# Kernel tuning notes

Measured on AMD Instinct MI355X. Metric: run time of the kernel, lower is better.

The kernel has to match this reference:

```python
import jax, jax.numpy as jnp
import numpy as np

B, L, CIN = 128, 2048, 38
D, S, PD, FEAT, FD, NH = 64, 32, 32, 64, 128, 4


def _ln(x, g, b, eps=1e-5):
    m = jnp.mean(x, axis=-1, keepdims=True)
    v = jnp.var(x, axis=-1, keepdims=True)
    return (x - m) / jnp.sqrt(v + eps) * g + b


def _gelu(x):
    return jax.nn.gelu(x, approximate=False)


def setup_inputs():
    key = jax.random.key(0)
    ks = jax.random.split(key, 20)
    w = lambda k, shape: jax.random.normal(k, shape, jnp.float32) * 0.02
    z = lambda *s: jnp.zeros(s, jnp.float32)
    inp = {}
    inp['x'] = jax.random.normal(ks[0], (B, L, CIN), jnp.float32)
    # physics core
    inp['Wv'] = w(ks[1], (3, CIN)); inp['bv'] = z(3)
    inp['Wr'] = w(ks[2], (3, CIN)); inp['br'] = z(3)
    inp['Wpe'] = w(ks[3], (5, PD)); inp['bpe'] = z(PD)
    inp['g_pe'] = jnp.ones((PD,), jnp.float32); inp['be_pe'] = z(PD)
    # mamba stream: in-proj + LN, then selective-scan block
    inp['Wmi'] = w(ks[4], (CIN, D)); inp['bmi'] = z(D)
    inp['g_m'] = jnp.ones((D,), jnp.float32); inp['b_m'] = z(D)
    inp['A_log'] = jnp.tile(jnp.log(jnp.arange(1, S + 1, dtype=jnp.float32)), (D, 1))
    inp['Wdt'] = w(ks[5], (1, D)); inp['bdt'] = z(D)
    inp['Wxp'] = w(ks[6], (D, 2 * S)); inp['bxp'] = z(2 * S)
    inp['Wmo'] = w(ks[7], (D, D)); inp['bmo'] = z(D)
    # champion feature extractor (stand-in: mean-pool + linear to champion_feat_dim)
    inp['Wch'] = w(ks[8], (CIN, FEAT)); inp['bch'] = z(FEAT)
    # alignment + attention fusion + classifier
    inp['Wac'] = w(ks[9], (FEAT, FD)); inp['bac'] = z(FD)
    inp['Wamp'] = w(ks[10], (PD + D, FD)); inp['bamp'] = z(FD)
    inp['Wq'] = w(ks[11], (FD, FD)); inp['bq'] = z(FD)
    inp['Wk'] = w(ks[12], (FD, FD)); inp['bk'] = z(FD)
    inp['Wva'] = w(ks[13], (FD, FD)); inp['bva'] = z(FD)
    inp['Wo'] = w(ks[14], (FD, FD)); inp['bo'] = z(FD)
    inp['Wc1'] = w(ks[15], (FD, 64)); inp['bc1'] = z(64)
    inp['Wc2'] = w(ks[16], (64, 1)); inp['bc2'] = z(1)
    return inp


def reference(x, Wv, bv, Wr, br, Wpe, bpe, g_pe, be_pe, Wmi, bmi, g_m, b_m,
              A_log, Wdt, bdt, Wxp, bxp, Wmo, bmo, Wch, bch, Wac, bac,
              Wamp, bamp, Wq, bq, Wk, bk, Wva, bva, Wo, bo, Wc1, bc1, Wc2, bc2):
    Bn, Ln, _ = x.shape
    # ---------- TulparPhysicsCore (conv1d k=1 == per-position linear) ----------
    v_vec = jnp.clip(jnp.einsum('blc,oc->blo', x, Wv) + bv, -15.0, 15.0)      # [B,L,3]
    r_vec = jnp.clip(jax.nn.softplus(jnp.einsum('blc,oc->blo', x, Wr) + br), 0.1, 3000.0)
    v_mag = jnp.linalg.norm(v_vec, axis=-1)                                    # [B,L]
    r_mag = jnp.linalg.norm(r_vec, axis=-1)
    energy = v_mag ** 2 / 2.0 - 1.0 / r_mag
    ediff = jnp.concatenate([jnp.zeros((Bn, 1), x.dtype), energy[:, 1:] - energy[:, :-1]], axis=1)
    praw = jnp.stack([v_mag, r_mag, energy, ediff, r_mag / v_mag], axis=-1)    # [B,L,5]
    phys = _gelu(_ln(praw @ Wpe + bpe, g_pe, be_pe))                           # [B,L,PD]
    # ---------- mamba stream: Linear -> LN -> GELU -> selective scan ----------
    h = _gelu(_ln(x @ Wmi + bmi, g_m, b_m))                                    # [B,L,D]
    A = -jnp.exp(A_log)                                                        # [D,S]
    dt = jax.nn.softplus(h[:, :, 0:1] @ Wdt + bdt)                             # [B,L,D]
    Bm, Cm = jnp.split(h @ Wxp + bxp, 2, axis=-1)                              # [B,L,S] each

    def step(state, inp_t):
        dt_t, h_t, B_t, C_t = inp_t                                            # [B,D],[B,D],[B,S],[B,S]
        dA = jnp.exp(A[None] * dt_t[:, :, None])                               # [B,D,S]
        state = dA * state + dt_t[:, :, None] * h_t[:, :, None] * B_t[:, None, :]
        y = (state * C_t[:, None, :]).sum(-1)                                  # [B,D]
        return state, y

    init = jnp.zeros((Bn, D, S), x.dtype)
    xs = (dt.transpose(1, 0, 2), h.transpose(1, 0, 2),
          Bm.transpose(1, 0, 2), Cm.transpose(1, 0, 2))
    _, ys = jax.lax.scan(step, init, xs)                                       # [L,B,D]
    mamba = ys.transpose(1, 0, 2) @ Wmo + bmo                                  # [B,L,D]
    # ---------- fusion ----------
    kv = jnp.concatenate([phys, mamba], axis=-1) @ Wamp + bamp                 # [B,L,FD]
    feat = x.mean(axis=1) @ Wch + bch                                          # [B,FEAT] (champion.get_features)
    q = (feat @ Wac + bac)[:, None, :]                                         # [B,1,FD]
    Dh = FD // NH
    qh = (q @ Wq + bq).reshape(Bn, 1, NH, Dh).transpose(0, 2, 1, 3)            # [B,H,1,Dh]
    kh = (kv @ Wk + bk).reshape(Bn, Ln, NH, Dh).transpose(0, 2, 1, 3)          # [B,H,L,Dh]
    vh = (kv @ Wva + bva).reshape(Bn, Ln, NH, Dh).transpose(0, 2, 1, 3)
    scores = jnp.einsum('bhqd,bhkd->bhqk', qh, kh) * (1.0 / np.sqrt(Dh))
    att = jax.nn.softmax(scores, axis=-1)                                      # [B,H,1,L]
    o = jnp.einsum('bhqk,bhkd->bhqd', att, vh).transpose(0, 2, 1, 3).reshape(Bn, 1, FD)
    o = (o @ Wo + bo)[:, 0, :]                                                 # [B,FD]
    # ---------- classifier (dropout = identity in eval) ----------
    return _gelu(o @ Wc1 + bc1) @ Wc2 + bc2                                    # [B,1]
```

## Files before the change

kernel.cpp:

```cpp
#include <hip/hip_runtime.h>
#include <math.h>

constexpr int B   = 128;
constexpr int L   = 2048;
constexpr int CIN = 38;
constexpr int D   = 64;
constexpr int S   = 32;
constexpr int PD  = 32;
constexpr int FEAT= 64;
constexpr int FD  = 128;
constexpr int NH  = 4;
constexpr int DH  = 32;

constexpr int NC  = 32;
constexpr int CL  = 64;
constexpr int TT  = 16;
constexpr int NCH = 16;
constexpr int CHL = 128;
constexpr int NBLK = (B*L)/64;

constexpr size_t SZ_H   = (size_t)B*L*D;
constexpr size_t SZ_BC  = (size_t)B*L*S;
constexpr size_t SZ_PH  = (size_t)B*L*PD;
constexpr size_t SZ_ST  = (size_t)B*NC*D*S;
constexpr size_t SZ_SDT = (size_t)B*NC*D;

constexpr size_t OFF_H    = 0;
constexpr size_t OFF_BC   = OFF_H   + SZ_H;
constexpr size_t OFF_CC   = OFF_BC  + SZ_BC;
constexpr size_t OFF_PHYS = OFF_CC  + SZ_BC;
constexpr size_t OFF_ST   = OFF_PHYS+ SZ_PH;
constexpr size_t OFF_SDT  = OFF_ST  + SZ_ST;
constexpr size_t OFF_XM   = OFF_SDT + SZ_SDT;
constexpr size_t OFF_PA   = OFF_XM  + (size_t)NBLK*CIN;
constexpr size_t OFF_PY   = OFF_PA  + (size_t)B*NH*PD;
constexpr size_t OFF_C0   = OFF_PY  + (size_t)B*NH*D;
constexpr size_t OFF_PMS  = OFF_ST;
constexpr size_t OFF_PCTX = OFF_ST + 32768;

__device__ __forceinline__ float fast_rcp(float v) {
#if __has_builtin(__builtin_amdgcn_rcpf)
    return __builtin_amdgcn_rcpf(v);
#else
    return 1.f / v;
#endif
}
__device__ __forceinline__ float sp_fast(float z) {
    return fmaxf(z, 0.f) + __logf(1.f + __expf(-fabsf(z)));
}
__device__ __forceinline__ float gelu_fast(float v) {
    const float u = v * 0.70710678118654752f;
    const float a = fabsf(u);
    const float t = fast_rcp(fmaf(0.3275911f, a, 1.f));
    const float poly = t*(0.254829592f + t*(-0.284496736f + t*(1.421413741f
                        + t*(-1.453152027f + t*1.061405429f))));
    const float e = __expf(-a*a);
    const float erfa = fmaf(-poly, e, 1.f);
    const float erfu = copysignf(erfa, u);
    return 0.5f * v * (1.f + erfu);
}

__device__ __forceinline__ float energy_at(const float* __restrict__ xr,
    const float* __restrict__ Wv, const float* __restrict__ bv,
    const float* __restrict__ Wr, const float* __restrict__ br)
{
    float vm2 = 0.f, rm2 = 0.f;
    #pragma unroll
    for (int o = 0; o < 3; o++) {
        float a = bv[o], rr = br[o];
        #pragma unroll
        for (int c = 0; c < CIN; c++) {
            a  = fmaf(xr[c], Wv[o*CIN + c], a);
            rr = fmaf(xr[c], Wr[o*CIN + c], rr);
        }
        a  = fminf(fmaxf(a, -15.f), 15.f);
        rr = fminf(fmaxf(sp_fast(rr), 0.1f), 3000.f);
        vm2 += a*a; rm2 += rr*rr;
    }
    const float rmag = sqrtf(rm2);
    return 0.5f*vm2 - 1.f/rmag;
}

__global__ __launch_bounds__(256, 6) void k_pre(
    const float* __restrict__ x,
    const float* __restrict__ Wv,  const float* __restrict__ bv,
    const float* __restrict__ Wr,  const float* __restrict__ br,
    const float* __restrict__ Wpe, const float* __restrict__ bpe,
    const float* __restrict__ gpe, const float* __restrict__ bepe,
    const float* __restrict__ Wmi, const float* __restrict__ bmi,
    const float* __restrict__ gm,  const float* __restrict__ bm,
    const float* __restrict__ Wxp, const float* __restrict__ bxp,
    float* __restrict__ hws, float* __restrict__ bcw,
    float* __restrict__ ccw, float* __restrict__ phw,
    float* __restrict__ xpart)
{
    __shared__ __align__(16) float smem[4928];
    const int tid = threadIdx.x;
    const int g   = __builtin_amdgcn_readfirstlane(tid) >> 6;
    const int row = tid & 63;
    const int r0  = blockIdx.x * 64;
    const int p   = r0 + row;
    const int l   = p & (L - 1);
    const float* xr = x + (size_t)p * CIN;

    float xv[CIN];
    #pragma unroll
    for (int c = 0; c < CIN; c++) xv[c] = xr[c];

    if (g == 0) {
        #pragma unroll
        for (int c = 0; c < CIN; c++) smem[row*40 + c] = xv[c];
    }
    __syncthreads();

    if (g == 0) {
        float vm2 = 0.f, rm2 = 0.f;
        #pragma unroll
        for (int o = 0; o < 3; o++) {
            float a = bv[o], rr = br[o];
            #pragma unroll
            for (int c = 0; c < CIN; c++) {
                a  = fmaf(xv[c], Wv[o*CIN + c], a);
                rr = fmaf(xv[c], Wr[o*CIN + c], rr);
            }
            a  = fminf(fmaxf(a, -15.f), 15.f);
            rr = fminf(fmaxf(sp_fast(rr), 0.1f), 3000.f);
            vm2 += a*a; rm2 += rr*rr;
        }
        const float vmag = sqrtf(vm2), rmag = sqrtf(rm2);
        const float energy = 0.5f*vm2 - 1.f/rmag;
        float eprev = __shfl(energy, (row == 0) ? 0 : row - 1, 64);
        if (row == 0 && l > 0) eprev = energy_at(xr - CIN, Wv, bv, Wr, br);
        const float ediff = (l == 0) ? 0.f : (energy - eprev);
        smem[2720 + row*5 + 0] = vmag;
        smem[2720 + row*5 + 1] = rmag;
        smem[2720 + row*5 + 2] = energy;
        smem[2720 + row*5 + 3] = ediff;
        smem[2720 + row*5 + 4] = rmag / vmag;
    }
    if (tid >= 128 && tid < 128 + 4*CIN) {
        const int idx = tid - 128;
        const int c2 = idx >> 2, sub = idx & 3;
        float s2 = 0.f;
        #pragma unroll
        for (int r2 = 0; r2 < 16; r2++) s2 += smem[(sub*16 + r2)*40 + c2];
        smem[3552 + idx] = s2;
    }
    __syncthreads();
    if (tid < CIN)
        xpart[(size_t)blockIdx.x*CIN + tid] = smem[3552 + 4*tid] + smem[3552 + 4*tid + 1]
                                            + smem[3552 + 4*tid + 2] + smem[3552 + 4*tid + 3];

    {
        float pr[5];
        #pragma unroll
        for (int j = 0; j < 5; j++) pr[j] = smem[2720 + row*5 + j];
        float peo[8]; float ls = 0.f, lq = 0.f;
        #pragma unroll
        for (int i = 0; i < 8; i++) {
            const int ii = 8*g + i;
            float a = bpe[ii];
            #pragma unroll
            for (int k = 0; k < 5; k++) a = fmaf(pr[k], Wpe[k*PD + ii], a);
            peo[i] = a; ls += a; lq += a*a;
        }
        smem[3040 + g*64 + row] = ls;
        smem[3296 + g*64 + row] = lq;
        __syncthreads();
        float mu = 0.f, sq = 0.f;
        #pragma unroll
        for (int w = 0; w < 4; w++) {
            mu += smem[3040 + w*64 + row];
            sq += smem[3296 + w*64 + row];
        }
        mu *= (1.f/PD);
        const float var = fmaxf(sq*(1.f/PD) - mu*mu, 0.f);
        const float rstd = rsqrtf(var + 1e-5f);
        #pragma unroll
        for (int k = 0; k < 2; k++) {
            float4 q;
            q.x = gelu_fast((peo[4*k+0]-mu)*rstd*gpe[8*g+4*k+0] + bepe[8*g+4*k+0]);
            q.y = gelu_fast((peo[4*k+1]-mu)*rstd*gpe[8*g+4*k+1] + bepe[8*g+4*k+1]);
            q.z = gelu_fast((peo[4*k+2]-mu)*rstd*gpe[8*g+4*k+2] + bepe[8*g+4*k+2]);
            q.w = gelu_fast((peo[4*k+3]-mu)*rstd*gpe[8*g+4*k+3] + bepe[8*g+4*k+3]);
            *(float4*)&smem[row*36 + 8*g + 4*k] = q;
        }
    }
    __syncthreads();
    {
        float* pb = phw + (size_t)r0 * PD;
        #pragma unroll
        for (int k = 0; k < 2; k++) {
            const int flat = k*1024 + tid*4;
            const int rr = flat >> 5, cc = flat & 31;
            *(float4*)&pb[flat] = *(const float4*)&smem[rr*36 + cc];
        }
    }
    __syncthreads();

    float hq[16];
    {
        float sum = 0.f, sumsq = 0.f;
        #pragma unroll
        for (int jj = 0; jj < 4; jj++) {
            #pragma unroll
            for (int j2 = 0; j2 < 4; j2++) {
                const int d = 16*g + 4*jj + j2;
                float a = bmi[d];
                #pragma unroll
                for (int c = 0; c < CIN; c++) a = fmaf(xv[c], Wmi[c*D + d], a);
                hq[4*jj + j2] = a; sum += a; sumsq += a*a;
            }
        }
        smem[4352 + g*64 + row] = sum;
        smem[4608 + g*64 + row] = sumsq;
    }
    __syncthreads();
    {
        float s = 0.f, sq = 0.f;
        #pragma unroll
        for (int w = 0; w < 4; w++) {
            s  += smem[4352 + w*64 + row];
            sq += smem[4608 + w*64 + row];
        }
        const float mu = s * (1.f/D);
        const float var = fmaxf(sq*(1.f/D) - mu*mu, 0.f);
        const float rstd = rsqrtf(var + 1e-5f);
        #pragma unroll
        for (int jj = 0; jj < 4; jj++) {
            const int d0 = 16*g + 4*jj;
            float4 q;
            q.x = gelu_fast(fmaf((hq[4*jj+0]-mu)*rstd, gm[d0+0], bm[d0+0]));
            q.y = gelu_fast(fmaf((hq[4*jj+1]-mu)*rstd, gm[d0+1], bm[d0+1]));
            q.z = gelu_fast(fmaf((hq[4*jj+2]-mu)*rstd, gm[d0+2], bm[d0+2]));
            q.w = gelu_fast(fmaf((hq[4*jj+3]-mu)*rstd, gm[d0+3], bm[d0+3]));
            *(float4*)&smem[row*68 + d0] = q;
        }
    }
    __syncthreads();
    {
        float* hb = hws + (size_t)r0 * D;
        #pragma unroll
        for (int k = 0; k < 4; k++) {
            const int flat = k*1024 + tid*4;
            const int rr = flat >> 6, cc = flat & 63;
            *(float4*)&hb[flat] = *(const float4*)&smem[rr*68 + cc];
        }
    }

    float acc[16];
    {
        const int j0 = 16*g;
        #pragma unroll
        for (int j = 0; j < 16; j++) acc[j] = bxp[j0 + j];
        #pragma unroll 1
        for (int dg = 0; dg < 16; dg++) {
            const float4 hv4 = *(const float4*)&smem[row*68 + 4*dg];
            const float hv[4] = {hv4.x, hv4.y, hv4.z, hv4.w};
            #pragma unroll
            for (int j2 = 0; j2 < 4; j2++) {
                const int d = 4*dg + j2;
                #pragma unroll
                for (int j = 0; j < 16; j++)
                    acc[j] = fmaf(hv[j2], Wxp[d*2*S + j0 + j], acc[j]);
            }
        }
    }
    __syncthreads();
    {
        float* dst = (g < 2) ? &smem[row*36 + 16*g] : &smem[2304 + row*36 + 16*(g-2)];
        #pragma unroll
        for (int k = 0; k < 4; k++)
            *(float4*)&dst[4*k] = make_float4(acc[4*k], acc[4*k+1], acc[4*k+2], acc[4*k+3]);
    }
    __syncthreads();
    {
        float* bb = bcw + (size_t)r0 * S;
        float* cb = ccw + (size_t)r0 * S;
        #pragma unroll
        for (int k = 0; k < 2; k++) {
            const int flat = k*1024 + tid*4;
            const int rr = flat >> 5, cc = flat & 31;
            *(float4*)&bb[flat] = *(const float4*)&smem[rr*36 + cc];
            *(float4*)&cb[flat] = *(const float4*)&smem[2304 + rr*36 + cc];
        }
    }
}

__global__ __launch_bounds__(64) void k_q(
    const float* __restrict__ xpart,
    const float* __restrict__ Wch, const float* __restrict__ bch,
    const float* __restrict__ Wac, const float* __restrict__ bac,
    const float* __restrict__ Wq,  const float* __restrict__ bq,
    const float* __restrict__ Wk,  const float* __restrict__ bk,
    const float* __restrict__ Wamp,const float* __restrict__ bamp,
    const float* __restrict__ Wmo, const float* __restrict__ bmo,
    float* __restrict__ pA, float* __restrict__ pY, float* __restrict__ c0w)
{
    const int bh = blockIdx.x;
    const int b = bh >> 2, h = bh & 3;
    const int t = threadIdx.x;
    __shared__ float xmL[CIN];
    __shared__ float featL[FEAT], qL[FD], qvL[FD], qkL[FD], pML[D];
    __shared__ float qbL;
    if (t < CIN) {
        float s2 = 0.f;
        #pragma unroll 4
        for (int g2 = 0; g2 < 32; g2++) s2 += xpart[((size_t)b*32 + g2)*CIN + t];
        xmL[t] = s2 * (1.f/L);
    }
    __syncthreads();
    {
        float a = bch[t];
        #pragma unroll
        for (int c = 0; c < CIN; c++) a = fmaf(xmL[c], Wch[c*FEAT + t], a);
        featL[t] = a;
    }
    __syncthreads();
    #pragma unroll
    for (int k2 = 0; k2 < 2; k2++) {
        const int f = t + k2*64;
        float a = bac[f];
        #pragma unroll
        for (int j = 0; j < FEAT; j++) a = fmaf(featL[j], Wac[j*FD + f], a);
        qL[f] = a;
    }
    __syncthreads();
    #pragma unroll
    for (int k2 = 0; k2 < 2; k2++) {
        const int f = t + k2*64;
        float a = bq[f];
        #pragma unroll
        for (int j = 0; j < FD; j++) a = fmaf(qL[j], Wq[j*FD + f], a);
        qvL[f] = a;
    }
    __syncthreads();
    #pragma unroll
    for (int k2 = 0; k2 < 2; k2++) {
        const int f = t + k2*64;
        float a = 0.f;
        #pragma unroll
        for (int j = 0; j < DH; j++) a = fmaf(Wk[f*FD + h*DH + j], qvL[h*DH + j], a);
        qkL[f] = a;
    }
    if (t == 0) {
        float a = 0.f;
        for (int j = 0; j < DH; j++) a = fmaf(bk[h*DH + j], qvL[h*DH + j], a);
        qbL = a;
    }
    __syncthreads();
    const float sc = 0.17677669529663688f;
    if (t < PD) {
        float a = 0.f;
        #pragma unroll
        for (int f = 0; f < FD; f++) a = fmaf(Wamp[t*FD + f], qkL[f], a);
        pA[bh*PD + t] = a * sc;
    }
    {
        float a = 0.f;
        #pragma unroll
        for (int f = 0; f < FD; f++) a = fmaf(Wamp[(PD + t)*FD + f], qkL[f], a);
        pML[t] = a;
    }
    __syncthreads();
    {
        float a = 0.f;
        #pragma unroll
        for (int d2 = 0; d2 < D; d2++) a = fmaf(Wmo[t*D + d2], pML[d2], a);
        pY[bh*D + t] = a * sc;
    }
    if (t == 0) {
        float a = qbL;
        for (int f = 0; f < FD; f++)  a = fmaf(bamp[f], qkL[f], a);
        for (int d2 = 0; d2 < D; d2++) a = fmaf(bmo[d2], pML[d2], a);
        c0w[bh] = a * sc;
    }
}

__global__ __launch_bounds__(256) void k_scan1(
    const float* __restrict__ Wdt, const float* __restrict__ bdt,
    const float* __restrict__ hws, const float* __restrict__ bcw,
    float* __restrict__ stw, float* __restrict__ sdtw)
{
    __shared__ __align__(16) float hL[TT*D];
    __shared__ __align__(16) float bL[TT*S];
    __shared__ __align__(16) float uL[TT*D];
    __shared__ __align__(16) float e1L[TT*D];
    __shared__ float sdL[4*D];
    const int bc = blockIdx.x;
    const int b = bc >> 5, c = bc & (NC - 1);
    const int tid = threadIdx.x;
    const int d = tid & 63, w = tid >> 6;
    const float wdt = Wdt[d], bd = bdt[d];
    float st[8];
    #pragma unroll
    for (int k = 0; k < 8; k++) st[k] = 0.f;
    float sumdt = 0.f;
    const size_t row0 = (size_t)b*L + (size_t)c*CL;
    const float* hg = hws + row0*D;
    const float* bg = bcw + row0*S;

    float4 hpre = *(const float4*)&hg[tid*4];
    float4 bpre;
    if (tid < 128) bpre = *(const float4*)&bg[tid*4];

    for (int ts = 0; ts < CL/TT; ts++) {
        *(float4*)&hL[tid*4] = hpre;
        if (tid < 128) *(float4*)&bL[tid*4] = bpre;
        __syncthreads();
        if (ts < CL/TT - 1) {
            hpre = *(const float4*)&hg[(ts+1)*TT*D + tid*4];
            if (tid < 128) bpre = *(const float4*)&bg[(ts+1)*TT*S + tid*4];
        }
        #pragma unroll
        for (int j = 0; j < 4; j++) {
            const int t = 4*w + j;
            const float h0 = hL[t*D];
            const float hd = hL[t*D + d];
            float z = fmaf(h0, wdt, bd);
            z = fminf(fmaxf(z, -30.f), 30.f);
            const float ez = __expf(z);
            const float e1 = fast_rcp(1.f + ez);
            const float dt = -__logf(e1);
            sumdt += dt;
            uL[t*D + d]  = dt * hd;
            e1L[t*D + d] = e1;
        }
        __syncthreads();
        #pragma unroll
        for (int t = 0; t < TT; t++) {
            const float e1 = e1L[t*D + d];
            const float u  = uL[t*D + d];
            const float e2 = e1*e1, e4 = e2*e2, e8 = e4*e4, e16 = e8*e8;
            float pf = e1;
            pf *= (w & 1) ? e8 : 1.f;
            pf *= (w & 2) ? e16 : 1.f;
            float bv[8];
            *(float4*)&bv[0] = *(const float4*)&bL[t*S + 8*w];
            *(float4*)&bv[4] = *(const float4*)&bL[t*S + 8*w + 4];
            #pragma unroll
            for (int k = 0; k < 8; k++) {
                st[k] = fmaf(pf, st[k], u * bv[k]);
                pf *= e1;
            }
        }
        __syncthreads();
    }
    float* F = stw + (size_t)bc*(D*S) + (size_t)(8*w)*D + d;
    #pragma unroll
    for (int k = 0; k < 8; k++) F[k*D] = st[k];
    sdL[w*D + d] = sumdt;
    __syncthreads();
    if (tid < D)
        sdtw[(size_t)bc*D + tid] = sdL[tid] + sdL[D + tid] + sdL[2*D + tid] + sdL[3*D + tid];
}

__global__ __launch_bounds__(256) void k_scan2(float* __restrict__ stw,
                                               const float* __restrict__ sdtw)
{
    const int idx = blockIdx.x*256 + threadIdx.x;
    const int d = idx & 63;
    const int s = (idx >> 6) & (S - 1);
    const int b = idx >> 11;
    const float sp1 = -(float)(s + 1);
    float st = 0.f;
    for (int c = 0; c < NC; c++) {
        float* p2 = stw + (size_t)(b*NC + c)*(D*S) + (size_t)s*D + d;
        const float sdt = sdtw[(size_t)(b*NC + c)*D + d];
        const float F = *p2;
        *p2 = st;
        st = fmaf(__expf(sp1 * sdt), st, F);
    }
}

__global__ __launch_bounds__(256) void k_scan3(
    const float* __restrict__ Wdt, const float* __restrict__ bdt,
    float* __restrict__ hws,
    const float* __restrict__ bcw, const float* __restrict__ ccw,
    const float* __restrict__ stw)
{
    __shared__ __align__(16) float hL[TT*D];
    __shared__ __align__(16) float bL[TT*S];
    __shared__ __align__(16) float cL[TT*S];
    __shared__ __align__(16) float uL[TT*D];
    __shared__ __align__(16) float e1L[TT*D];
    __shared__ __align__(16) float ypL[4*TT*D];
    const int bc = blockIdx.x;
    const int b = bc >> 5, c = bc & (NC - 1);
    const int tid = threadIdx.x;
    const int d = tid & 63, w = tid >> 6;
    const float wdt = Wdt[d], bd = bdt[d];
    float st[8];
    {
        const float* initp = stw + (size_t)bc*(D*S) + (size_t)(8*w)*D + d;
        #pragma unroll
        for (int k = 0; k < 8; k++) st[k] = initp[k*D];
    }
    const size_t row0 = (size_t)b*L + (size_t)c*CL;
    float* hg = hws + row0*D;
    const float* bg = bcw + row0*S;
    const float* cg = ccw + row0*S;

    float4 hpre = *(const float4*)&hg[tid*4];
    float4 bcpre;
    if (tid < 128) bcpre = *(const float4*)&bg[tid*4];
    else           bcpre = *(const float4*)&cg[(tid-128)*4];

    for (int ts = 0; ts < CL/TT; ts++) {
        *(float4*)&hL[tid*4] = hpre;
        if (tid < 128) *(float4*)&bL[tid*4] = bcpre;
        else           *(float4*)&cL[(tid-128)*4] = bcpre;
        __syncthreads();
        if (ts < CL/TT - 1) {
            hpre = *(const float4*)&hg[(ts+1)*TT*D + tid*4];
            if (tid < 128) bcpre = *(const float4*)&bg[(ts+1)*TT*S + tid*4];
            else           bcpre = *(const float4*)&cg[(ts+1)*TT*S + (tid-128)*4];
        }
        #pragma unroll
        for (int j = 0; j < 4; j++) {
            const int t = 4*w + j;
            const float h0 = hL[t*D];
            const float hd = hL[t*D + d];
            float z = fmaf(h0, wdt, bd);
            z = fminf(fmaxf(z, -30.f), 30.f);
            const float ez = __expf(z);
            const float e1 = fast_rcp(1.f + ez);
            const float dt = -__logf(e1);
            uL[t*D + d]  = dt * hd;
            e1L[t*D + d] = e1;
        }
        __syncthreads();
        #pragma unroll
        for (int t = 0; t < TT; t++) {
            const float e1 = e1L[t*D + d];
            const float u  = uL[t*D + d];
            const float e2 = e1*e1, e4 = e2*e2, e8 = e4*e4, e16 = e8*e8;
            float pf = e1;
            pf *= (w & 1) ? e8 : 1.f;
            pf *= (w & 2) ? e16 : 1.f;
            float bv[8], cv[8];
            *(float4*)&bv[0] = *(const float4*)&bL[t*S + 8*w];
            *(float4*)&bv[4] = *(const float4*)&bL[t*S + 8*w + 4];
            *(float4*)&cv[0] = *(const float4*)&cL[t*S + 8*w];
            *(float4*)&cv[4] = *(const float4*)&cL[t*S + 8*w + 4];
            float y = 0.f;
            #pragma unroll
            for (int k = 0; k < 8; k++) {
                st[k] = fmaf(pf, st[k], u * bv[k]);
                y = fmaf(st[k], cv[k], y);
                pf *= e1;
            }
            ypL[(w*TT + t)*D + d] = y;
        }
        __syncthreads();
        {
            const int flat = tid*4;
            float4 a  = *(const float4*)&ypL[flat];
            const float4 p1 = *(const float4*)&ypL[TT*D + flat];
            const float4 p2 = *(const float4*)&ypL[2*TT*D + flat];
            const float4 p3 = *(const float4*)&ypL[3*TT*D + flat];
            a.x += p1.x + p2.x + p3.x;
            a.y += p1.y + p2.y + p3.y;
            a.z += p1.z + p2.z + p3.z;
            a.w += p1.w + p2.w + p3.w;
            *(float4*)&hg[(size_t)(ts*TT)*D + flat] = a;
        }
        __syncthreads();
    }
}

__global__ __launch_bounds__(256) void k_att(
    const float* __restrict__ phw, const float* __restrict__ yw,
    const float* __restrict__ pA,  const float* __restrict__ pY,
    const float* __restrict__ c0w,
    float* __restrict__ pms, float* __restrict__ pctx)
{
    const int blk = blockIdx.x;
    const int b = blk >> 4, c = blk & (NCH - 1);
    const int tid = threadIdx.x;
    __shared__ __align__(16) float phL[CHL*36];
    __shared__ __align__(16) float yL[CHL*68];
    __shared__ float scL[NH*CHL];
    __shared__ float wL[CHL*NH];
    __shared__ __align__(16) float sPA[NH*PD];
    __shared__ __align__(16) float sPY[NH*D];
    __shared__ float sC0[NH];

    if (tid < NH*PD) sPA[tid] = pA[(size_t)b*NH*PD + tid];
    sPY[tid] = pY[(size_t)b*NH*D + tid];
    if (tid < NH) sC0[tid] = c0w[b*NH + tid];

    const float* phg = phw + ((size_t)b*L + (size_t)c*CHL)*PD;
    #pragma unroll
    for (int it = 0; it < 4; it++) {
        const int flat = it*1024 + tid*4;
        const int row = flat >> 5, col = flat & 31;
        *(float4*)&phL[row*36 + col] = *(const float4*)&phg[flat];
    }
    const float* yg = yw + ((size_t)b*L + (size_t)c*CHL)*D;
    #pragma unroll
    for (int it = 0; it < 8; it++) {
        const int flat = it*1024 + tid*4;
        const int row = flat >> 6, col = flat & 63;
        *(float4*)&yL[row*68 + col] = *(const float4*)&yg[flat];
    }
    __syncthreads();

    #pragma unroll
    for (int it = 0; it < 2; it++) {
        const int item = it*256 + tid;
        const int row = item & (CHL - 1), hh = item >> 7;
        float a = sC0[hh];
        #pragma unroll
        for (int k = 0; k < 8; k++) {
            const float4 pq = *(const float4*)&phL[row*36 + 4*k];
            const float4 aq = *(const float4*)&sPA[hh*PD + 4*k];
            a = fmaf(pq.x, aq.x, a); a = fmaf(pq.y, aq.y, a);
            a = fmaf(pq.z, aq.z, a); a = fmaf(pq.w, aq.w, a);
        }
        #pragma unroll
        for (int k = 0; k < 16; k++) {
            const float4 yq = *(const float4*)&yL[row*68 + 4*k];
            const float4 aq = *(const float4*)&sPY[hh*D + 4*k];
            a = fmaf(yq.x, aq.x, a); a = fmaf(yq.y, aq.y, a);
            a = fmaf(yq.z, aq.z, a); a = fmaf(yq.w, aq.w, a);
        }
        scL[hh*CHL + row] = a;
    }
    __syncthreads();

    {
        const int hh = tid >> 6, lane = tid & 63;
        const float v0 = scL[hh*CHL + lane], v1 = scL[hh*CHL + lane + 64];
        float mx = fmaxf(v0, v1);
        #pragma unroll
        for (int o = 32; o > 0; o >>= 1) mx = fmaxf(mx, __shfl_xor(mx, o, 64));
        const float e0 = __expf(v0 - mx), e1 = __expf(v1 - mx);
        wL[lane*NH + hh] = e0;
        wL[(lane + 64)*NH + hh] = e1;
        float sum = e0 + e1;
        #pragma unroll
        for (int o = 32; o > 0; o >>= 1) sum += __shfl_xor(sum, o, 64);
        if (lane == 0) {
            pms[((size_t)blk*NH + hh)*2 + 0] = mx;
            pms[((size_t)blk*NH + hh)*2 + 1] = sum;
        }
    }
    __syncthreads();

    for (int item = tid; item < NH*(PD + D); item += 256) {
        const int hh = item / (PD + D), e = item % (PD + D);
        const float* fb; int stp;
        if (e < PD) { fb = &phL[e]; stp = 36; }
        else        { fb = &yL[e - PD]; stp = 68; }
        float acc = 0.f;
        #pragma unroll 4
        for (int r = 0; r < CHL; r++) acc = fmaf(wL[r*NH + hh], fb[r*stp], acc);
        pctx[((size_t)blk*NH + hh)*(PD + D) + e] = acc;
    }
}

__global__ __launch_bounds__(128) void k_att2(
    const float* __restrict__ pms, const float* __restrict__ pctx,
    const float* __restrict__ Wmo, const float* __restrict__ bmo,
    const float* __restrict__ Wamp,const float* __restrict__ bamp,
    const float* __restrict__ Wva, const float* __restrict__ bva,
    const float* __restrict__ Wo,  const float* __restrict__ bo,
    const float* __restrict__ Wc1, const float* __restrict__ bc1,
    const float* __restrict__ Wc2, const float* __restrict__ bc2,
    float* __restrict__ out)
{
    const int b = blockIdx.x, t = threadIdx.x;
    __shared__ float ctxL[NH][PD + D];
    __shared__ float catL[NH][PD + D];
    __shared__ float ckvL[NH][FD];
    __shared__ float oL[FD], ooL[FD], c1L[64];

    for (int idx = t; idx < NH*(PD + D); idx += 128) {
        const int hh = idx / (PD + D), e = idx % (PD + D);
        float M = -3.0e38f;
        for (int cc = 0; cc < NCH; cc++)
            M = fmaxf(M, pms[((size_t)(b*NCH + cc)*NH + hh)*2]);
        float Ssum = 0.f, acc = 0.f;
        for (int cc = 0; cc < NCH; cc++) {
            const size_t pi = (size_t)(b*NCH + cc)*NH + hh;
            const float f = __expf(pms[pi*2] - M);
            Ssum += pms[pi*2 + 1] * f;
            acc  += f * pctx[pi*(PD + D) + e];
        }
        ctxL[hh][e] = acc / Ssum;
    }
    __syncthreads();
    for (int idx = t; idx < NH*(PD + D); idx += 128) {
        const int hh = idx / (PD + D), i = idx % (PD + D);
        float a;
        if (i < PD) a = ctxL[hh][i];
        else {
            const int d2 = i - PD;
            a = bmo[d2];
            #pragma unroll
            for (int e = 0; e < D; e++) a = fmaf(ctxL[hh][PD + e], Wmo[e*D + d2], a);
        }
        catL[hh][i] = a;
    }
    __syncthreads();
    for (int idx = t; idx < NH*FD; idx += 128) {
        const int hh = idx / FD, f = idx % FD;
        float a = bamp[f];
        #pragma unroll
        for (int i = 0; i < PD + D; i++) a = fmaf(catL[hh][i], Wamp[i*FD + f], a);
        ckvL[hh][f] = a;
    }
    __syncthreads();
    {
        const int hh = t / DH, j = t % DH;
        float a = bva[hh*DH + j];
        #pragma unroll
        for (int f = 0; f < FD; f++) a = fmaf(ckvL[hh][f], Wva[f*FD + hh*DH + j], a);
        oL[t] = a;
    }
    __syncthreads();
    {
        float a = bo[t];
        #pragma unroll
        for (int f = 0; f < FD; f++) a = fmaf(oL[f], Wo[f*FD + t], a);
        ooL[t] = a;
    }
    __syncthreads();
    if (t < 64) {
        float a = bc1[t];
        #pragma unroll
        for (int f = 0; f < FD; f++) a = fmaf(ooL[f], Wc1[f*64 + t], a);
        c1L[t] = gelu_fast(a);
    }
    __syncthreads();
    if (t == 0) {
        float a = bc2[0];
        for (int k2 = 0; k2 < 64; k2++) a = fmaf(c1L[k2], Wc2[k2], a);
        out[b] = a;
    }
}

extern "C" void kernel_launch(void* const* d_in, const int* in_sizes, int n_in,
                              void* d_out, int out_size, void* d_ws, size_t ws_size,
                              hipStream_t stream)
{
    const float* x    = (const float*)d_in[0];
    const float* Wv   = (const float*)d_in[1];
    const float* bv   = (const float*)d_in[2];
    const float* Wr   = (const float*)d_in[3];
    const float* br   = (const float*)d_in[4];
    const float* Wpe  = (const float*)d_in[5];
    const float* bpe  = (const float*)d_in[6];
    const float* gpe  = (const float*)d_in[7];
    const float* bepe = (const float*)d_in[8];
    const float* Wmi  = (const float*)d_in[9];
    const float* bmi  = (const float*)d_in[10];
    const float* gm   = (const float*)d_in[11];
    const float* bm   = (const float*)d_in[12];
    const float* Wdt  = (const float*)d_in[14];
    const float* bdt  = (const float*)d_in[15];
    const float* Wxp  = (const float*)d_in[16];
    const float* bxp  = (const float*)d_in[17];
    const float* Wmo  = (const float*)d_in[18];
    const float* bmo  = (const float*)d_in[19];
    const float* Wch  = (const float*)d_in[20];
    const float* bch  = (const float*)d_in[21];
    const float* Wac  = (const float*)d_in[22];
    const float* bac  = (const float*)d_in[23];
    const float* Wamp = (const float*)d_in[24];
    const float* bamp = (const float*)d_in[25];
    const float* Wq   = (const float*)d_in[26];
    const float* bq   = (const float*)d_in[27];
    const float* Wk   = (const float*)d_in[28];
    const float* bk   = (const float*)d_in[29];
    const float* Wva  = (const float*)d_in[30];
    const float* bva  = (const float*)d_in[31];
    const float* Wo   = (const float*)d_in[32];
    const float* bo   = (const float*)d_in[33];
    const float* Wc1  = (const float*)d_in[34];
    const float* bc1  = (const float*)d_in[35];
    const float* Wc2  = (const float*)d_in[36];
    const float* bc2  = (const float*)d_in[37];

    float* ws  = (float*)d_ws;
    float* out = (float*)d_out;

    float* hws  = ws + OFF_H;
    float* bcw  = ws + OFF_BC;
    float* ccw  = ws + OFF_CC;
    float* phw  = ws + OFF_PHYS;
    float* stw  = ws + OFF_ST;
    float* sdtw = ws + OFF_SDT;
    float* xmw  = ws + OFF_XM;
    float* pAw  = ws + OFF_PA;
    float* pYw  = ws + OFF_PY;
    float* c0w  = ws + OFF_C0;
    float* pms  = ws + OFF_PMS;
    float* pctx = ws + OFF_PCTX;

    k_pre<<<dim3(NBLK), dim3(256), 0, stream>>>(x, Wv, bv, Wr, br, Wpe, bpe,
        gpe, bepe, Wmi, bmi, gm, bm, Wxp, bxp, hws, bcw, ccw, phw, xmw);
    k_q<<<dim3(B*NH), dim3(64), 0, stream>>>(xmw, Wch, bch, Wac, bac, Wq, bq,
        Wk, bk, Wamp, bamp, Wmo, bmo, pAw, pYw, c0w);
    k_scan1<<<dim3(B*NC), dim3(256), 0, stream>>>(Wdt, bdt, hws, bcw, stw, sdtw);
    k_scan2<<<dim3((B*S*D)/256), dim3(256), 0, stream>>>(stw, sdtw);
    k_scan3<<<dim3(B*NC), dim3(256), 0, stream>>>(Wdt, bdt, hws, bcw, ccw, stw);
    k_att<<<dim3(B*NCH), dim3(256), 0, stream>>>(phw, hws, pAw, pYw, c0w, pms, pctx);
    k_att2<<<dim3(B), dim3(128), 0, stream>>>(pms, pctx, Wmo, bmo, Wamp, bamp,
        Wva, bva, Wo, bo, Wc1, bc1, Wc2, bc2, out);
}
```

Measured before the change: 459.6 us.

## Fuse chunk-state scan into preprocessing and fuse output scan with attention

```diff
diff --git a/kernel.cpp b/kernel.cpp
--- a/kernel.cpp
+++ b/kernel.cpp
@@ -35,8 +35,6 @@
 constexpr size_t OFF_PA   = OFF_XM  + (size_t)NBLK*CIN;
 constexpr size_t OFF_PY   = OFF_PA  + (size_t)B*NH*PD;
 constexpr size_t OFF_C0   = OFF_PY  + (size_t)B*NH*D;
-constexpr size_t OFF_PMS  = OFF_ST;
-constexpr size_t OFF_PCTX = OFF_ST + 32768;
 
 __device__ __forceinline__ float fast_rcp(float v) {
 #if __has_builtin(__builtin_amdgcn_rcpf)
@@ -81,7 +79,7 @@
     return 0.5f*vm2 - 1.f/rmag;
 }
 
-__global__ __launch_bounds__(256, 6) void k_pre(
+__global__ __launch_bounds__(256, 4) void k_pre(
     const float* __restrict__ x,
     const float* __restrict__ Wv,  const float* __restrict__ bv,
     const float* __restrict__ Wr,  const float* __restrict__ br,
@@ -90,11 +88,15 @@
     const float* __restrict__ Wmi, const float* __restrict__ bmi,
     const float* __restrict__ gm,  const float* __restrict__ bm,
     const float* __restrict__ Wxp, const float* __restrict__ bxp,
+    const float* __restrict__ Wdt, const float* __restrict__ bdt,
     float* __restrict__ hws, float* __restrict__ bcw,
     float* __restrict__ ccw, float* __restrict__ phw,
-    float* __restrict__ xpart)
+    float* __restrict__ xpart, float* __restrict__ stw,
+    float* __restrict__ sdtw)
 {
-    __shared__ __align__(16) float smem[4928];
+    __shared__ __align__(16) float smem[9216];
+    constexpr int TB0 = 4352, TC0 = 6656;
+    constexpr int PH36 = 4352, PR0 = 6656, PS0 = 6976, PQ0 = 7232, XMP = 8960;
     const int tid = threadIdx.x;
     const int g   = __builtin_amdgcn_readfirstlane(tid) >> 6;
     const int row = tid & 63;
@@ -132,11 +134,11 @@
         float eprev = __shfl(energy, (row == 0) ? 0 : row - 1, 64);
         if (row == 0 && l > 0) eprev = energy_at(xr - CIN, Wv, bv, Wr, br);
         const float ediff = (l == 0) ? 0.f : (energy - eprev);
-        smem[2720 + row*5 + 0] = vmag;
-        smem[2720 + row*5 + 1] = rmag;
-        smem[2720 + row*5 + 2] = energy;
-        smem[2720 + row*5 + 3] = ediff;
-        smem[2720 + row*5 + 4] = rmag / vmag;
+        smem[PR0 + row*5 + 0] = vmag;
+        smem[PR0 + row*5 + 1] = rmag;
+        smem[PR0 + row*5 + 2] = energy;
+        smem[PR0 + row*5 + 3] = ediff;
+        smem[PR0 + row*5 + 4] = rmag / vmag;
     }
     if (tid >= 128 && tid < 128 + 4*CIN) {
         const int idx = tid - 128;
@@ -144,17 +146,17 @@
         float s2 = 0.f;
         #pragma unroll
         for (int r2 = 0; r2 < 16; r2++) s2 += smem[(sub*16 + r2)*40 + c2];
-        smem[3552 + idx] = s2;
+        smem[XMP + idx] = s2;
     }
     __syncthreads();
     if (tid < CIN)
-        xpart[(size_t)blockIdx.x*CIN + tid] = smem[3552 + 4*tid] + smem[3552 + 4*tid + 1]
-                                            + smem[3552 + 4*tid + 2] + smem[3552 + 4*tid + 3];
+        xpart[(size_t)blockIdx.x*CIN + tid] = smem[XMP + 4*tid] + smem[XMP + 4*tid + 1]
+                                            + smem[XMP + 4*tid + 2] + smem[XMP + 4*tid + 3];
 
     {
         float pr[5];
         #pragma unroll
-        for (int j = 0; j < 5; j++) pr[j] = smem[2720 + row*5 + j];
+        for (int j = 0; j < 5; j++) pr[j] = smem[PR0 + row*5 + j];
         float peo[8]; float ls = 0.f, lq = 0.f;
         #pragma unroll
         for (int i = 0; i < 8; i++) {
@@ -164,14 +166,14 @@
             for (int k = 0; k < 5; k++) a = fmaf(pr[k], Wpe[k*PD + ii], a);
             peo[i] = a; ls += a; lq += a*a;
         }
-        smem[3040 + g*64 + row] = ls;
-        smem[3296 + g*64 + row] = lq;
+        smem[PS0 + g*64 + row] = ls;
+        smem[PQ0 + g*64 + row] = lq;
         __syncthreads();
         float mu = 0.f, sq = 0.f;
         #pragma unroll
         for (int w = 0; w < 4; w++) {
-            mu += smem[3040 + w*64 + row];
-            sq += smem[3296 + w*64 + row];
+            mu += smem[PS0 + w*64 + row];
+            sq += smem[PQ0 + w*64 + row];
         }
         mu *= (1.f/PD);
         const float var = fmaxf(sq*(1.f/PD) - mu*mu, 0.f);
@@ -183,7 +185,7 @@
             q.y = gelu_fast((peo[4*k+1]-mu)*rstd*gpe[8*g+4*k+1] + bepe[8*g+4*k+1]);
             q.z = gelu_fast((peo[4*k+2]-mu)*rstd*gpe[8*g+4*k+2] + bepe[8*g+4*k+2]);
             q.w = gelu_fast((peo[4*k+3]-mu)*rstd*gpe[8*g+4*k+3] + bepe[8*g+4*k+3]);
-            *(float4*)&smem[row*36 + 8*g + 4*k] = q;
+            *(float4*)&smem[PH36 + row*36 + 8*g + 4*k] = q;
         }
     }
     __syncthreads();
@@ -193,7 +195,7 @@
         for (int k = 0; k < 2; k++) {
             const int flat = k*1024 + tid*4;
             const int rr = flat >> 5, cc = flat & 31;
-            *(float4*)&pb[flat] = *(const float4*)&smem[rr*36 + cc];
+            *(float4*)&pb[flat] = *(const float4*)&smem[PH36 + rr*36 + cc];
         }
     }
     __syncthreads();
@@ -212,16 +214,16 @@
                 hq[4*jj + j2] = a; sum += a; sumsq += a*a;
             }
         }
-        smem[4352 + g*64 + row] = sum;
-        smem[4608 + g*64 + row] = sumsq;
+        smem[PS0 + g*64 + row] = sum;
+        smem[PQ0 + g*64 + row] = sumsq;
     }
     __syncthreads();
     {
         float s = 0.f, sq = 0.f;
         #pragma unroll
         for (int w = 0; w < 4; w++) {
-            s  += smem[4352 + w*64 + row];
-            sq += smem[4608 + w*64 + row];
+            s  += smem[PS0 + w*64 + row];
+            sq += smem[PQ0 + w*64 + row];
         }
         const float mu = s * (1.f/D);
         const float var = fmaxf(sq*(1.f/D) - mu*mu, 0.f);
@@ -266,9 +268,8 @@
             }
         }
     }
-    __syncthreads();
-    {
-        float* dst = (g < 2) ? &smem[row*36 + 16*g] : &smem[2304 + row*36 + 16*(g-2)];
+    {
+        float* dst = (g < 2) ? &smem[TB0 + row*36 + 16*g] : &smem[TC0 + row*36 + 16*(g-2)];
         #pragma unroll
         for (int k = 0; k < 4; k++)
             *(float4*)&dst[4*k] = make_float4(acc[4*k], acc[4*k+1], acc[4*k+2], acc[4*k+3]);
@@ -281,9 +282,45 @@
         for (int k = 0; k < 2; k++) {
             const int flat = k*1024 + tid*4;
             const int rr = flat >> 5, cc = flat & 31;
-            *(float4*)&bb[flat] = *(const float4*)&smem[rr*36 + cc];
-            *(float4*)&cb[flat] = *(const float4*)&smem[2304 + rr*36 + cc];
-        }
+            *(float4*)&bb[flat] = *(const float4*)&smem[TB0 + rr*36 + cc];
+            *(float4*)&cb[flat] = *(const float4*)&smem[TC0 + rr*36 + cc];
+        }
+    }
+
+    {
+        const float wdt = Wdt[row], bd2 = bdt[row];
+        float st[8];
+        #pragma unroll
+        for (int k = 0; k < 8; k++) st[k] = 0.f;
+        float sumdt = 0.f;
+        #pragma unroll 2
+        for (int t = 0; t < CL; t++) {
+            const float h0 = smem[t*68];
+            const float hd = smem[t*68 + row];
+            float z = fmaf(h0, wdt, bd2);
+            z = fminf(fmaxf(z, -30.f), 30.f);
+            const float ez = __expf(z);
+            const float e1 = fast_rcp(1.f + ez);
+            const float dt = -__logf(e1);
+            sumdt += dt;
+            const float u = dt * hd;
+            const float e2 = e1*e1, e4 = e2*e2, e8 = e4*e4, e16 = e8*e8;
+            float pf = e1;
+            pf *= (g & 1) ? e8 : 1.f;
+            pf *= (g & 2) ? e16 : 1.f;
+            float bvv[8];
+            *(float4*)&bvv[0] = *(const float4*)&smem[TB0 + t*36 + 8*g];
+            *(float4*)&bvv[4] = *(const float4*)&smem[TB0 + t*36 + 8*g + 4];
+            #pragma unroll
+            for (int k = 0; k < 8; k++) {
+                st[k] = fmaf(pf, st[k], u * bvv[k]);
+                pf *= e1;
+            }
+        }
+        float* F = stw + (size_t)blockIdx.x*(D*S) + (size_t)(8*g)*D + row;
+        #pragma unroll
+        for (int k = 0; k < 8; k++) F[k*D] = st[k];
+        if (g == 0) sdtw[(size_t)blockIdx.x*D + row] = sumdt;
     }
 }
 
@@ -377,84 +414,6 @@
     }
 }
 
-__global__ __launch_bounds__(256) void k_scan1(
-    const float* __restrict__ Wdt, const float* __restrict__ bdt,
-    const float* __restrict__ hws, const float* __restrict__ bcw,
-    float* __restrict__ stw, float* __restrict__ sdtw)
-{
-    __shared__ __align__(16) float hL[TT*D];
-    __shared__ __align__(16) float bL[TT*S];
-    __shared__ __align__(16) float uL[TT*D];
-    __shared__ __align__(16) float e1L[TT*D];
-    __shared__ float sdL[4*D];
-    const int bc = blockIdx.x;
-    const int b = bc >> 5, c = bc & (NC - 1);
-    const int tid = threadIdx.x;
-    const int d = tid & 63, w = tid >> 6;
-    const float wdt = Wdt[d], bd = bdt[d];
-    float st[8];
-    #pragma unroll
-    for (int k = 0; k < 8; k++) st[k] = 0.f;
-    float sumdt = 0.f;
-    const size_t row0 = (size_t)b*L + (size_t)c*CL;
-    const float* hg = hws + row0*D;
-    const float* bg = bcw + row0*S;
-
-    float4 hpre = *(const float4*)&hg[tid*4];
-    float4 bpre;
-    if (tid < 128) bpre = *(const float4*)&bg[tid*4];
-
-    for (int ts = 0; ts < CL/TT; ts++) {
-        *(float4*)&hL[tid*4] = hpre;
-        if (tid < 128) *(float4*)&bL[tid*4] = bpre;
-        __syncthreads();
-        if (ts < CL/TT - 1) {
-            hpre = *(const float4*)&hg[(ts+1)*TT*D + tid*4];
-            if (tid < 128) bpre = *(const float4*)&bg[(ts+1)*TT*S + tid*4];
-        }
-        #pragma unroll
-        for (int j = 0; j < 4; j++) {
-            const int t = 4*w + j;
-            const float h0 = hL[t*D];
-            const float hd = hL[t*D + d];
-            float z = fmaf(h0, wdt, bd);
-            z = fminf(fmaxf(z, -30.f), 30.f);
-            const float ez = __expf(z);
-            const float e1 = fast_rcp(1.f + ez);
-            const float dt = -__logf(e1);
-            sumdt += dt;
-            uL[t*D + d]  = dt * hd;
-            e1L[t*D + d] = e1;
-        }
-        __syncthreads();
-        #pragma unroll
-        for (int t = 0; t < TT; t++) {
-            const float e1 = e1L[t*D + d];
-            const float u  = uL[t*D + d];
-            const float e2 = e1*e1, e4 = e2*e2, e8 = e4*e4, e16 = e8*e8;
-            float pf = e1;
-            pf *= (w & 1) ? e8 : 1.f;
-            pf *= (w & 2) ? e16 : 1.f;
-            float bv[8];
-            *(float4*)&bv[0] = *(const float4*)&bL[t*S + 8*w];
-            *(float4*)&bv[4] = *(const float4*)&bL[t*S + 8*w + 4];
-            #pragma unroll
-            for (int k = 0; k < 8; k++) {
-                st[k] = fmaf(pf, st[k], u * bv[k]);
-                pf *= e1;
-            }
-        }
-        __syncthreads();
-    }
-    float* F = stw + (size_t)bc*(D*S) + (size_t)(8*w)*D + d;
-    #pragma unroll
-    for (int k = 0; k < 8; k++) F[k*D] = st[k];
-    sdL[w*D + d] = sumdt;
-    __syncthreads();
-    if (tid < D)
-        sdtw[(size_t)bc*D + tid] = sdL[tid] + sdL[D + tid] + sdL[2*D + tid] + sdL[3*D + tid];
-}
-
 __global__ __launch_bounds__(256) void k_scan2(float* __restrict__ stw,
                                                const float* __restrict__ sdtw)
 {
@@ -473,52 +432,66 @@
     }
 }
 
-__global__ __launch_bounds__(256) void k_scan3(
+__global__ __launch_bounds__(256, 4) void k_scan3att(
     const float* __restrict__ Wdt, const float* __restrict__ bdt,
-    float* __restrict__ hws,
-    const float* __restrict__ bcw, const float* __restrict__ ccw,
-    const float* __restrict__ stw)
+    const float* __restrict__ hws, const float* __restrict__ bcw,
+    const float* __restrict__ ccw, const float* __restrict__ phw,
+    const float* __restrict__ pA,  const float* __restrict__ pY,
+    const float* __restrict__ c0w, float* __restrict__ stw)
 {
     __shared__ __align__(16) float hL[TT*D];
     __shared__ __align__(16) float bL[TT*S];
     __shared__ __align__(16) float cL[TT*S];
-    __shared__ __align__(16) float uL[TT*D];
-    __shared__ __align__(16) float e1L[TT*D];
     __shared__ __align__(16) float ypL[4*TT*D];
-    const int bc = blockIdx.x;
-    const int b = bc >> 5, c = bc & (NC - 1);
+    __shared__ __align__(16) float ySub[TT*68];
+    __shared__ __align__(16) float phSub[TT*36];
+    __shared__ float wSub[64];
+    __shared__ float mh[NH], lh[NH], alphaL[NH];
+    __shared__ __align__(16) float sPA[NH*PD];
+    __shared__ __align__(16) float sPY[NH*D];
+    __shared__ float sC0[NH];
+    const int blk = blockIdx.x;
+    const int b = blk >> 4, c = blk & (NCH - 1);
     const int tid = threadIdx.x;
     const int d = tid & 63, w = tid >> 6;
     const float wdt = Wdt[d], bd = bdt[d];
     float st[8];
     {
-        const float* initp = stw + (size_t)bc*(D*S) + (size_t)(8*w)*D + d;
+        const float* initp = stw + (size_t)(b*NC + 2*c)*(D*S) + (size_t)(8*w)*D + d;
         #pragma unroll
         for (int k = 0; k < 8; k++) st[k] = initp[k*D];
     }
-    const size_t row0 = (size_t)b*L + (size_t)c*CL;
-    float* hg = hws + row0*D;
+    if (tid < NH*PD) sPA[tid] = pA[(size_t)b*NH*PD + tid];
+    sPY[tid] = pY[(size_t)b*NH*D + tid];
+    if (tid < NH) { sC0[tid] = c0w[b*NH + tid]; mh[tid] = -3.0e38f; lh[tid] = 0.f; }
+    float acc0 = 0.f, acc1 = 0.f;
+    const size_t row0 = (size_t)b*L + (size_t)c*CHL;
+    const float* hg = hws + row0*D;
     const float* bg = bcw + row0*S;
     const float* cg = ccw + row0*S;
-
+    const float* pg = phw + row0*PD;
     float4 hpre = *(const float4*)&hg[tid*4];
-    float4 bcpre;
-    if (tid < 128) bcpre = *(const float4*)&bg[tid*4];
-    else           bcpre = *(const float4*)&cg[(tid-128)*4];
-
-    for (int ts = 0; ts < CL/TT; ts++) {
+    float4 bcpre = (tid < 128) ? *(const float4*)&bg[tid*4]
+                               : *(const float4*)&cg[(tid-128)*4];
+    float2 ppre = *(const float2*)&pg[tid*2];
+
+    for (int ts = 0; ts < CHL/TT; ts++) {
         *(float4*)&hL[tid*4] = hpre;
         if (tid < 128) *(float4*)&bL[tid*4] = bcpre;
         else           *(float4*)&cL[(tid-128)*4] = bcpre;
+        {
+            const int flat = tid*2;
+            *(float2*)&phSub[(flat >> 5)*36 + (flat & 31)] = ppre;
+        }
         __syncthreads();
-        if (ts < CL/TT - 1) {
+        if (ts < CHL/TT - 1) {
             hpre = *(const float4*)&hg[(ts+1)*TT*D + tid*4];
-            if (tid < 128) bcpre = *(const float4*)&bg[(ts+1)*TT*S + tid*4];
-            else           bcpre = *(const float4*)&cg[(ts+1)*TT*S + (tid-128)*4];
-        }
-        #pragma unroll
-        for (int j = 0; j < 4; j++) {
-            const int t = 4*w + j;
+            bcpre = (tid < 128) ? *(const float4*)&bg[(ts+1)*TT*S + tid*4]
+                                : *(const float4*)&cg[(ts+1)*TT*S + (tid-128)*4];
+            ppre = *(const float2*)&pg[(ts+1)*TT*PD + tid*2];
+        }
+        #pragma unroll 2
+        for (int t = 0; t < TT; t++) {
             const float h0 = hL[t*D];
             const float hd = hL[t*D + d];
             float z = fmaf(h0, wdt, bd);
@@ -526,14 +499,7 @@
             const float ez = __expf(z);
             const float e1 = fast_rcp(1.f + ez);
             const float dt = -__logf(e1);
-            uL[t*D + d]  = dt * hd;
-            e1L[t*D + d] = e1;
-        }
-        __syncthreads();
-        #pragma unroll
-        for (int t = 0; t < TT; t++) {
-            const float e1 = e1L[t*D + d];
-            const float u  = uL[t*D + d];
+            const float u = dt * hd;
             const float e2 = e1*e1, e4 = e2*e2, e8 = e4*e4, e16 = e8*e8;
             float pf = e1;
             pf *= (w & 1) ? e8 : 1.f;
@@ -555,6 +521,7 @@
         __syncthreads();
         {
             const int flat = tid*4;
+            const int r = flat >> 6, col = flat & 63;
             float4 a  = *(const float4*)&ypL[flat];
             const float4 p1 = *(const float4*)&ypL[TT*D + flat];
             const float4 p2 = *(const float4*)&ypL[2*TT*D + flat];
@@ -563,105 +530,75 @@
             a.y += p1.y + p2.y + p3.y;
             a.z += p1.z + p2.z + p3.z;
             a.w += p1.w + p2.w + p3.w;
-            *(float4*)&hg[(size_t)(ts*TT)*D + flat] = a;
+            *(float4*)&ySub[r*68 + col] = a;
         }
         __syncthreads();
-    }
-}
-
-__global__ __launch_bounds__(256) void k_att(
-    const float* __restrict__ phw, const float* __restrict__ yw,
-    const float* __restrict__ pA,  const float* __restrict__ pY,
-    const float* __restrict__ c0w,
-    float* __restrict__ pms, float* __restrict__ pctx)
-{
-    const int blk = blockIdx.x;
-    const int b = blk >> 4, c = blk & (NCH - 1);
-    const int tid = threadIdx.x;
-    __shared__ __align__(16) float phL[CHL*36];
-    __shared__ __align__(16) float yL[CHL*68];
-    __shared__ float scL[NH*CHL];
-    __shared__ float wL[CHL*NH];
-    __shared__ __align__(16) float sPA[NH*PD];
-    __shared__ __align__(16) float sPY[NH*D];
-    __shared__ float sC0[NH];
-
-    if (tid < NH*PD) sPA[tid] = pA[(size_t)b*NH*PD + tid];
-    sPY[tid] = pY[(size_t)b*NH*D + tid];
-    if (tid < NH) sC0[tid] = c0w[b*NH + tid];
-
-    const float* phg = phw + ((size_t)b*L + (size_t)c*CHL)*PD;
-    #pragma unroll
-    for (int it = 0; it < 4; it++) {
-        const int flat = it*1024 + tid*4;
-        const int row = flat >> 5, col = flat & 31;
-        *(float4*)&phL[row*36 + col] = *(const float4*)&phg[flat];
-    }
-    const float* yg = yw + ((size_t)b*L + (size_t)c*CHL)*D;
-    #pragma unroll
-    for (int it = 0; it < 8; it++) {
-        const int flat = it*1024 + tid*4;
-        const int row = flat >> 6, col = flat & 63;
-        *(float4*)&yL[row*68 + col] = *(const float4*)&yg[flat];
-    }
-    __syncthreads();
-
-    #pragma unroll
-    for (int it = 0; it < 2; it++) {
-        const int item = it*256 + tid;
-        const int row = item & (CHL - 1), hh = item >> 7;
-        float a = sC0[hh];
-        #pragma unroll
-        for (int k = 0; k < 8; k++) {
-            const float4 pq = *(const float4*)&phL[row*36 + 4*k];
-            const float4 aq = *(const float4*)&sPA[hh*PD + 4*k];
-            a = fmaf(pq.x, aq.x, a); a = fmaf(pq.y, aq.y, a);
-            a = fmaf(pq.z, aq.z, a); a = fmaf(pq.w, aq.w, a);
-        }
-        #pragma unroll
-        for (int k = 0; k < 16; k++) {
-            const float4 yq = *(const float4*)&yL[row*68 + 4*k];
-            const float4 aq = *(const float4*)&sPY[hh*D + 4*k];
-            a = fmaf(yq.x, aq.x, a); a = fmaf(yq.y, aq.y, a);
-            a = fmaf(yq.z, aq.z, a); a = fmaf(yq.w, aq.w, a);
-        }
-        scL[hh*CHL + row] = a;
-    }
-    __syncthreads();
-
-    {
-        const int hh = tid >> 6, lane = tid & 63;
-        const float v0 = scL[hh*CHL + lane], v1 = scL[hh*CHL + lane + 64];
-        float mx = fmaxf(v0, v1);
-        #pragma unroll
-        for (int o = 32; o > 0; o >>= 1) mx = fmaxf(mx, __shfl_xor(mx, o, 64));
-        const float e0 = __expf(v0 - mx), e1 = __expf(v1 - mx);
-        wL[lane*NH + hh] = e0;
-        wL[(lane + 64)*NH + hh] = e1;
-        float sum = e0 + e1;
-        #pragma unroll
-        for (int o = 32; o > 0; o >>= 1) sum += __shfl_xor(sum, o, 64);
-        if (lane == 0) {
-            pms[((size_t)blk*NH + hh)*2 + 0] = mx;
-            pms[((size_t)blk*NH + hh)*2 + 1] = sum;
-        }
-    }
-    __syncthreads();
-
-    for (int item = tid; item < NH*(PD + D); item += 256) {
-        const int hh = item / (PD + D), e = item % (PD + D);
-        const float* fb; int stp;
-        if (e < PD) { fb = &phL[e]; stp = 36; }
-        else        { fb = &yL[e - PD]; stp = 68; }
-        float acc = 0.f;
-        #pragma unroll 4
-        for (int r = 0; r < CHL; r++) acc = fmaf(wL[r*NH + hh], fb[r*stp], acc);
-        pctx[((size_t)blk*NH + hh)*(PD + D) + e] = acc;
-    }
+        if (tid < 64) {
+            const int r = tid & 15, hh = tid >> 4;
+            float v = sC0[hh];
+            #pragma unroll
+            for (int k = 0; k < 8; k++) {
+                const float4 pq = *(const float4*)&phSub[r*36 + 4*k];
+                const float4 aq = *(const float4*)&sPA[hh*PD + 4*k];
+                v = fmaf(pq.x, aq.x, v); v = fmaf(pq.y, aq.y, v);
+                v = fmaf(pq.z, aq.z, v); v = fmaf(pq.w, aq.w, v);
+            }
+            #pragma unroll
+            for (int k = 0; k < 16; k++) {
+                const float4 yq = *(const float4*)&ySub[r*68 + 4*k];
+                const float4 aq = *(const float4*)&sPY[hh*D + 4*k];
+                v = fmaf(yq.x, aq.x, v); v = fmaf(yq.y, aq.y, v);
+                v = fmaf(yq.z, aq.z, v); v = fmaf(yq.w, aq.w, v);
+            }
+            float mx = v;
+            #pragma unroll
+            for (int o = 1; o < 16; o <<= 1) mx = fmaxf(mx, __shfl_xor(mx, o, 64));
+            const float mold = mh[hh];
+            const float mnew = fmaxf(mold, mx);
+            const float al = __expf(mold - mnew);
+            const float wv = __expf(v - mnew);
+            float ls = wv;
+            #pragma unroll
+            for (int o = 1; o < 16; o <<= 1) ls += __shfl_xor(ls, o, 64);
+            wSub[hh*16 + r] = wv;
+            if (r == 0) {
+                mh[hh] = mnew;
+                lh[hh] = lh[hh]*al + ls;
+                alphaL[hh] = al;
+            }
+        }
+        __syncthreads();
+        {
+            const int hh0 = tid / 96, e0 = tid - hh0*96;
+            const float al0 = alphaL[hh0];
+            const float* f0 = (e0 < PD) ? &phSub[e0] : &ySub[e0 - PD];
+            const int stp0 = (e0 < PD) ? 36 : 68;
+            float s0 = 0.f;
+            #pragma unroll 4
+            for (int r = 0; r < TT; r++) s0 = fmaf(wSub[hh0*16 + r], f0[r*stp0], s0);
+            acc0 = fmaf(acc0, al0, s0);
+            if (tid < 128) {
+                const int it = 256 + tid;
+                const int hh1 = it / 96, ei = it - hh1*96;
+                const float al1 = alphaL[hh1];
+                const float* f1 = (ei < PD) ? &phSub[ei] : &ySub[ei - PD];
+                const int stp1 = (ei < PD) ? 36 : 68;
+                float s1 = 0.f;
+                #pragma unroll 4
+                for (int r = 0; r < TT; r++) s1 = fmaf(wSub[hh1*16 + r], f1[r*stp1], s1);
+                acc1 = fmaf(acc1, al1, s1);
+            }
+        }
+        __syncthreads();
+    }
+    float* outp = stw + (size_t)(b*NC + 2*c + 1)*(D*S);
+    outp[tid] = acc0;
+    if (tid < 128) outp[256 + tid] = acc1;
+    if (tid < NH) { outp[384 + tid*2] = mh[tid]; outp[385 + tid*2] = lh[tid]; }
 }
 
 __global__ __launch_bounds__(128) void k_att2(
-    const float* __restrict__ pms, const float* __restrict__ pctx,
+    const float* __restrict__ pcw,
     const float* __restrict__ Wmo, const float* __restrict__ bmo,
     const float* __restrict__ Wamp,const float* __restrict__ bamp,
     const float* __restrict__ Wva, const float* __restrict__ bva,
@@ -680,13 +617,13 @@
         const int hh = idx / (PD + D), e = idx % (PD + D);
         float M = -3.0e38f;
         for (int cc = 0; cc < NCH; cc++)
-            M = fmaxf(M, pms[((size_t)(b*NCH + cc)*NH + hh)*2]);
+            M = fmaxf(M, pcw[(size_t)(b*NC + 2*cc + 1)*(D*S) + 384 + hh*2]);
         float Ssum = 0.f, acc = 0.f;
         for (int cc = 0; cc < NCH; cc++) {
-            const size_t pi = (size_t)(b*NCH + cc)*NH + hh;
-            const float f = __expf(pms[pi*2] - M);
-            Ssum += pms[pi*2 + 1] * f;
-            acc  += f * pctx[pi*(PD + D) + e];
+            const float* base = pcw + (size_t)(b*NC + 2*cc + 1)*(D*S);
+            const float f = __expf(base[384 + hh*2] - M);
+            Ssum += base[385 + hh*2] * f;
+            acc  += f * base[hh*96 + e];
         }
         ctxL[hh][e] = acc / Ssum;
     }
@@ -796,17 +733,15 @@
     float* pAw  = ws + OFF_PA;
     float* pYw  = ws + OFF_PY;
     float* c0w  = ws + OFF_C0;
-    float* pms  = ws + OFF_PMS;
-    float* pctx = ws + OFF_PCTX;
 
     k_pre<<<dim3(NBLK), dim3(256), 0, stream>>>(x, Wv, bv, Wr, br, Wpe, bpe,
-        gpe, bepe, Wmi, bmi, gm, bm, Wxp, bxp, hws, bcw, ccw, phw, xmw);
+        gpe, bepe, Wmi, bmi, gm, bm, Wxp, bxp, Wdt, bdt,
+        hws, bcw, ccw, phw, xmw, stw, sdtw);
     k_q<<<dim3(B*NH), dim3(64), 0, stream>>>(xmw, Wch, bch, Wac, bac, Wq, bq,
         Wk, bk, Wamp, bamp, Wmo, bmo, pAw, pYw, c0w);
-    k_scan1<<<dim3(B*NC), dim3(256), 0, stream>>>(Wdt, bdt, hws, bcw, stw, sdtw);
     k_scan2<<<dim3((B*S*D)/256), dim3(256), 0, stream>>>(stw, sdtw);
-    k_scan3<<<dim3(B*NC), dim3(256), 0, stream>>>(Wdt, bdt, hws, bcw, ccw, stw);
-    k_att<<<dim3(B*NCH), dim3(256), 0, stream>>>(phw, hws, pAw, pYw, c0w, pms, pctx);
-    k_att2<<<dim3(B), dim3(128), 0, stream>>>(pms, pctx, Wmo, bmo, Wamp, bamp,
+    k_scan3att<<<dim3(B*NCH), dim3(256), 0, stream>>>(Wdt, bdt, hws, bcw, ccw,
+        phw, pAw, pYw, c0w, stw);
+    k_att2<<<dim3(B), dim3(128), 0, stream>>>(stw, Wmo, bmo, Wamp, bamp,
         Wva, bva, Wo, bo, Wc1, bc1, Wc2, bc2, out);
 }
```

Measured after the change: 473.2 us. 1.03x slower.
